# Optimization experiments

Measured on AMD Instinct MI355X. Metric: run time of the kernel, lower is better.

The kernel has to match this reference:

```python
import jax, jax.numpy as jnp
import numpy as np


def _ifft2c(k):
    # centered orthonormal 2D inverse FFT over axes (0, 1)
    return jnp.fft.fftshift(
        jnp.fft.ifft2(jnp.fft.ifftshift(k, axes=(0, 1)), axes=(0, 1), norm='ortho'),
        axes=(0, 1))


def _warp_adjoint(im, flow):
    # Adjoint (transpose) of bilinear-interpolation motion matrix built from a
    # 2D displacement field: scatter-add each pixel's value to the 4 bilinear
    # neighbors of its displaced location (x+u, y+v).
    # im: [Nx, Ny] complex64, flow: [Nx, Ny, 2] float32
    Nx, Ny = im.shape
    X, Y = jnp.meshgrid(jnp.arange(Nx, dtype=flow.dtype),
                        jnp.arange(Ny, dtype=flow.dtype), indexing='ij')
    px = jnp.clip(X + flow[..., 0], 0.0, Nx - 1.0)
    py = jnp.clip(Y + flow[..., 1], 0.0, Ny - 1.0)
    x0 = jnp.floor(px).astype(jnp.int32)
    y0 = jnp.floor(py).astype(jnp.int32)
    x1 = jnp.minimum(x0 + 1, Nx - 1)
    y1 = jnp.minimum(y0 + 1, Ny - 1)
    wx = px - x0.astype(px.dtype)
    wy = py - y0.astype(py.dtype)
    out = jnp.zeros(Nx * Ny, dtype=im.dtype)
    for xi, yi, w in ((x0, y0, (1 - wx) * (1 - wy)),
                      (x0, y1, (1 - wx) * wy),
                      (x1, y0, wx * (1 - wy)),
                      (x1, y1, wx * wy)):
        out = out.at[(xi * Ny + yi).ravel()].add((w * im).ravel())
    return out.reshape(Nx, Ny)


def setup_inputs() -> dict:
    key = jax.random.key(0)
    k1, k2, k3, k4, k5, k6 = jax.random.split(key, 6)
    Nx, Ny, Nc, Nt = 320, 320, 16, 25
    kspace_r = jax.random.normal(k1, (Nx, Ny, Nc), dtype=jnp.float32)
    kspace_i = jax.random.normal(k2, (Nx, Ny, Nc), dtype=jnp.float32)
    # binary undersampling mask per coil per frame
    mask = jnp.round(jax.random.uniform(k3, (Nx, Ny, Nc, Nt), dtype=jnp.float32))
    smaps_r = jax.random.normal(k4, (Nx, Ny, Nc), dtype=jnp.float32)
    smaps_i = jax.random.normal(k5, (Nx, Ny, Nc), dtype=jnp.float32)
    # displacement fields, a few pixels of motion
    flow = 3.0 * jax.random.normal(k6, (Nx, Ny, 2, Nt), dtype=jnp.float32)
    return {'kspace_r': kspace_r, 'kspace_i': kspace_i, 'mask': mask,
            'smaps_r': smaps_r, 'smaps_i': smaps_i, 'flow': flow}


def reference(kspace_r, kspace_i, mask, smaps_r, smaps_i, flow):
    kspace = jax.lax.complex(kspace_r, kspace_i)          # [Nx,Ny,Nc]
    smaps = jax.lax.complex(smaps_r, smaps_i)             # [Nx,Ny,Nc]
    # per-frame masked k-space -> per-coil images: [Nx,Ny,Nc,Nt]
    km = kspace[:, :, :, None] * mask.astype(kspace.dtype)
    coil_ims = _ifft2c(km)
    # coil combine with conjugate sensitivities: [Nx,Ny,Nt]
    im_aux = jnp.sum(coil_ims * jnp.conj(smaps)[:, :, :, None], axis=2)
    # adjoint motion warp per frame, then sum over frames
    ims_t = jnp.moveaxis(im_aux, -1, 0)                   # [Nt,Nx,Ny]
    flows_t = jnp.moveaxis(flow, -1, 0)                   # [Nt,Nx,Ny,2]
    warped = jax.vmap(_warp_adjoint)(ims_t, flows_t)      # [Nt,Nx,Ny]
    out = jnp.sum(warped, axis=0)                         # [Nx,Ny] complex
    return jnp.stack([out.real, out.imag], axis=-1)       # [Nx,Ny,2] float32
```

## Files before the change

kernel.cpp:

```cpp
#include <hip/hip_runtime.h>
#include <hip/hip_fp16.h>


#define NX 320
#define NT 25
#define NC 16
#define BR 32
#define WH 16
static const float INV320 = 1.0f / 320.0f;

typedef float v2f __attribute__((ext_vector_type(2)));
typedef unsigned int u32;

__device__ __forceinline__ int rev6(int l) {
  return ((l & 1) << 5) | ((l & 2) << 3) | ((l & 4) << 1) |
         ((l & 8) >> 1) | ((l & 16) >> 3) | ((l & 32) >> 5);
}

__device__ __forceinline__ u32 h2u(__half2 h) {
  return *reinterpret_cast<u32*>(&h);
}
__device__ __forceinline__ __half2 u2h(u32 u) {
  return *reinterpret_cast<__half2*>(&u);
}
__device__ __forceinline__ __half2 swap16(__half2 h) {
  u32 u = h2u(h);
  u = (u >> 16) | (u << 16);
  return u2h(u);
}

template <int M>
__device__ __forceinline__ u32 lxoru(u32 x) {
  if constexpr (M == 1) {
    return (u32)__builtin_amdgcn_mov_dpp((int)x, 0xB1, 0xF, 0xF, true);
  } else if constexpr (M == 2) {
    return (u32)__builtin_amdgcn_mov_dpp((int)x, 0x4E, 0xF, 0xF, true);
  } else if constexpr (M == 32) {
    return (u32)__shfl_xor((int)x, 32);
  } else {
    constexpr int pat = (M << 10) | 0x1F;
    return (u32)__builtin_amdgcn_ds_swizzle((int)x, pat);
  }
}

struct TwH {
  __half2 sg[5], c2[5], s2n[5];
  __half2 sg5;
  __half2 w5c[4], w5s[4];
  __half2 C1h, C2h, S1h, nS1h, S2h, NP;
};

__device__ __forceinline__ void make_twh(int lane, TwH& tw) {
#pragma unroll
  for (int st = 0; st < 5; ++st) {
    int m = 32 >> st;
    bool bot = (lane & m) != 0;
    int j = lane & (m - 1);
    float ang = 3.14159265358979323846f * (float)j / (float)m;
    float s, c;
    __sincosf(ang, &s, &c);
    float g = bot ? -1.f : 1.f;
    float cc = bot ? c : 1.f, ss = bot ? s : 0.f;
    tw.sg[st] = __floats2half2_rn(g, g);
    tw.c2[st] = __floats2half2_rn(cc, cc);
    tw.s2n[st] = __floats2half2_rn(-ss, ss);
  }
  float g5 = (lane & 1) ? -1.f : 1.f;
  tw.sg5 = __floats2half2_rn(g5, g5);
  int k1 = rev6(lane);
  float b = (6.283185307179586f / 320.0f) * (float)k1;
  float s1, c1;
  __sincosf(b, &s1, &c1);
  float cq = 1.f, sq = 0.f;
#pragma unroll
  for (int q = 1; q < 5; ++q) {
    float nc = cq * c1 - sq * s1, ns = cq * s1 + sq * c1;
    cq = nc;
    sq = ns;
    tw.w5c[q - 1] = __floats2half2_rn(cq, cq);
    tw.w5s[q - 1] = __floats2half2_rn(-sq, sq);
  }
  const float C1 = 0.30901699437494742f, S1 = 0.95105651629515357f;
  const float C2 = -0.80901699437494742f, S2 = 0.58778525229247312f;
  tw.C1h = __floats2half2_rn(C1, C1);
  tw.C2h = __floats2half2_rn(C2, C2);
  tw.S1h = __floats2half2_rn(S1, S1);
  tw.nS1h = __floats2half2_rn(-S1, -S1);
  tw.S2h = __floats2half2_rn(S2, S2);
  tw.NP = __floats2half2_rn(-1.f, 1.f);
}

__device__ __forceinline__ __half2 cmul_h(__half2 t, __half2 c2, __half2 s2n) {
  return __hfma2(s2n, swap16(t), __hmul2(c2, t));
}

template <int M>
__device__ __forceinline__ void bstage_h(__half2 z[5], __half2 sg, __half2 c2,
                                         __half2 s2n) {
#pragma unroll
  for (int q = 0; q < 5; ++q) {
    __half2 o = u2h(lxoru<M>(h2u(z[q])));
    __half2 t = __hfma2(sg, z[q], o);
    z[q] = cmul_h(t, c2, s2n);
  }
}

__device__ __forceinline__ void fft320h(__half2 z[5], const TwH& tw) {
  bstage_h<32>(z, tw.sg[0], tw.c2[0], tw.s2n[0]);
  bstage_h<16>(z, tw.sg[1], tw.c2[1], tw.s2n[1]);
  bstage_h<8>(z, tw.sg[2], tw.c2[2], tw.s2n[2]);
  bstage_h<4>(z, tw.sg[3], tw.c2[3], tw.s2n[3]);
  bstage_h<2>(z, tw.sg[4], tw.c2[4], tw.s2n[4]);
  {
    __half2 o = u2h(lxoru<1>(h2u(z[0])));
    z[0] = __hfma2(tw.sg5, z[0], o);
#pragma unroll
    for (int q = 1; q < 5; ++q) {
      o = u2h(lxoru<1>(h2u(z[q])));
      __half2 t = __hfma2(tw.sg5, z[q], o);
      z[q] = cmul_h(t, tw.w5c[q - 1], tw.w5s[q - 1]);
    }
  }
  __half2 t0 = z[0], t1 = z[1], t2 = z[2], t3 = z[3], t4 = z[4];
  __half2 a1 = __hadd2(t1, t4), b1 = __hsub2(t1, t4);
  __half2 a2 = __hadd2(t2, t3), b2 = __hsub2(t2, t3);
  z[0] = __hadd2(t0, __hadd2(a1, a2));
  __half2 p = __hfma2(tw.C2h, a2, __hfma2(tw.C1h, a1, t0));
  __half2 q_ = __hfma2(tw.S2h, b2, __hmul2(tw.S1h, b1));
  __half2 r = __hfma2(tw.C1h, a2, __hfma2(tw.C2h, a1, t0));
  __half2 u = __hfma2(tw.nS1h, b2, __hmul2(tw.S2h, b1));
  __half2 qi = __hmul2(tw.NP, swap16(q_));
  __half2 ui = __hmul2(tw.NP, swap16(u));
  z[1] = __hadd2(p, qi);
  z[4] = __hsub2(p, qi);
  z[2] = __hadd2(r, ui);
  z[3] = __hsub2(r, ui);
}

__global__ __launch_bounds__(256) void prep_k(
    const float* __restrict__ mask, const float* __restrict__ kr,
    const float* __restrict__ ki, const float* __restrict__ sr,
    const float* __restrict__ si, const float* __restrict__ fl,
    unsigned int* __restrict__ mp, float2* __restrict__ kT,
    __half2* __restrict__ sT, float2* __restrict__ fs,
    float* __restrict__ out_f) {
  __shared__ __align__(16) char shmem[7552];
  int bid = blockIdx.x, tid = threadIdx.x;
  if (bid < 6400) {
    int xt = bid / 320, y = bid % 320;
    int w = tid >> 6, lane = tid & 63;
    float4* stage4 = (float4*)shmem;
    float* stage = (float*)shmem;
    unsigned int* tileu = (unsigned int*)(shmem + 6400);
#pragma unroll
    for (int k = 0; k < 4; ++k) {
      int xx = w * 4 + k;
      const float4* src =
          (const float4*)(mask + ((size_t)((xt * 16 + xx) * NX) + y) * (NC * NT));
      float4* dst4 = stage4 + w * 100;
      if (lane < 50) {
        dst4[lane] = src[lane];
        dst4[lane + 50] = src[lane + 50];
      }
      if (lane < 16) {
        const float* row = stage + w * 400 + lane * NT;
        unsigned int bits = 0;
#pragma unroll
        for (int t = 0; t < NT; ++t) bits |= (row[t] != 0.f) ? (1u << t) : 0u;
        tileu[xx * 17 + lane] = bits;
      }
    }
    __syncthreads();
    int c2 = tid >> 4, xx2 = tid & 15;
    mp[((size_t)(c2 * NX + y)) * NX + xt * 16 + xx2] = tileu[xx2 * 17 + c2];
  } else if (bid < 12800) {
    int r = bid - 6400;
    int xt = r % 20, y = r / 20;
    int xx = tid >> 4, c = tid & 15;
    float2* tilef = (float2*)shmem;
    size_t si_ = (size_t)((xt * 16 + xx) * NX + y) * NC + c;
    tilef[xx * 17 + c] = make_float2(kr[si_], ki[si_]);
    __syncthreads();
    int c2 = tid >> 4, xx2 = tid & 15;
    kT[((size_t)(c2 * NX + y)) * NX + xt * 16 + xx2] = tilef[xx2 * 17 + c2];
  } else if (bid < 19200) {
    int r = bid - 12800;
    int yt = r % 20, x = r / 20;
    int yy = tid >> 4, c = tid & 15;
    float2* tiles = (float2*)shmem;
    size_t si_ = (size_t)(x * NX + yt * 16 + yy) * NC + c;
    tiles[yy * 17 + c] = make_float2(sr[si_], si[si_]);
    __syncthreads();
    int c2 = tid >> 4, yy2 = tid & 15;
    float2 v = tiles[yy2 * 17 + c2];
    float sg = (yy2 & 1) ? -1.f : 1.f;
    sT[((size_t)(c2 * NX + x)) * NX + yt * 16 + yy2] =
        __floats2half2_rn(v.x * sg, v.y * sg);
  } else if (bid < 22400) {
    int r = bid - 19200;
    int nyt = r % 10, nx = r / 10;
    float* buf = (float*)shmem;
    size_t base = (size_t)(nx * NX + nyt * 32) * (2 * NT);
    const float2* src2 = (const float2*)(fl + base);
    float2* buf2 = (float2*)shmem;
    for (int f = tid; f < 800; f += 256) buf2[f] = src2[f];
    __syncthreads();
    for (int f = tid; f < 1600; f += 256) {
      int t = f / 64;
      int k = f % 64;
      int nyl = k >> 1, d = k & 1;
      size_t di = ((size_t)(t * NX + nx) * NX + nyt * 32 + nyl) * 2 + d;
      ((float*)fs)[di] = buf[(nyl * 2 + d) * NT + t];
    }
  } else {
    int idx = (bid - 22400) * 256 + tid;
    ((float4*)out_f)[idx] = make_float4(0.f, 0.f, 0.f, 0.f);
  }
}

__global__ __launch_bounds__(256) void pass1_k(
    const float2* __restrict__ kT, const unsigned int* __restrict__ mp,
    __half2* __restrict__ tmp, int c0) {
  int y = blockIdx.x, cg = blockIdx.y, c = c0 + cg;
  int tid = threadIdx.x, lane = tid & 63, w = tid >> 6;
  __half2 v[5];
  unsigned int mb[5];
  size_t rowbase = ((size_t)c * NX + y) * NX;
#pragma unroll
  for (int q = 0; q < 5; ++q) {
    int x = 5 * lane + q;
    float2 kv = kT[rowbase + x];
    float sg = ((lane + q) & 1) ? -INV320 : INV320;
    v[q] = __floats2half2_rn(kv.x * sg, kv.y * sg);
    mb[q] = mp[rowbase + x];
  }
  TwH tw;
  make_twh(lane, tw);
  int r6 = rev6(lane);
  float osg = ((lane & 32) ? -1.f : 1.f) * ((y & 1) ? -1.f : 1.f);
  __half2 osg2 = __floats2half2_rn(osg, osg);
  for (int t = w; t < NT; t += 4) {
    __half2 z[5];
#pragma unroll
    for (int q = 0; q < 5; ++q)
      z[q] = u2h(((mb[q] >> t) & 1u) ? h2u(v[q]) : 0u);
    fft320h(z, tw);
    __half2* dst = tmp + ((size_t)(cg * NT + t) * NX + y) * NX;
#pragma unroll
    for (int k2 = 0; k2 < 5; ++k2) dst[r6 + 64 * k2] = __hmul2(osg2, z[k2]);
  }
}

__global__ __launch_bounds__(256) void pass2_k(
    const __half2* __restrict__ tmp, const __half2* __restrict__ sT,
    __half2* __restrict__ im_aux, int c0, int G, int first) {
  int bx = blockIdx.x, t = blockIdx.y;
  int nxt_ = (bx >> 3) + 10 * (bx & 7);
  int tid = threadIdx.x, lane = tid & 63, j = tid >> 6;
  int nx = nxt_ * 4 + j;
  int k1 = rev6(lane);
  TwH tw;
  make_twh(lane, tw);
  __shared__ __half2 tile[2][NX][5];
  v2f acc[5] = {{0, 0}, {0, 0}, {0, 0}, {0, 0}, {0, 0}};

  int off[5], lw[5];
#pragma unroll
  for (int q = 0; q < 5; ++q) {
    int f = tid + q * 256;
    off[q] = (f >> 2) * NX + (f & 3);
    lw[q] = (f >> 2) * 5 + (f & 3);
  }
  const size_t pstride = (size_t)NT * NX * NX;
  const __half2* sbase = tmp + (size_t)t * NX * NX + nxt_ * 4;
  __half2* lds = &tile[0][0][0];

  __half2 nb[5];
#pragma unroll
  for (int q = 0; q < 5; ++q) nb[q] = sbase[off[q]];

  for (int cg = 0; cg < G; ++cg) {
    __half2 cb[5];
#pragma unroll
    for (int q = 0; q < 5; ++q) cb[q] = nb[q];
    if (cg + 1 < G) {
      const __half2* s = sbase + (size_t)(cg + 1) * pstride;
#pragma unroll
      for (int q = 0; q < 5; ++q) nb[q] = s[off[q]];
    }
    __half2* buf = lds + (cg & 1) * (NX * 5);
#pragma unroll
    for (int q = 0; q < 5; ++q) buf[lw[q]] = cb[q];
    const __half2* srow = sT + ((size_t)(c0 + cg) * NX + nx) * NX;
    __half2 smh[5];
#pragma unroll
    for (int k2 = 0; k2 < 5; ++k2) smh[k2] = srow[k1 + 64 * k2];
    __syncthreads();
    __half2 z[5];
#pragma unroll
    for (int q = 0; q < 5; ++q) z[q] = buf[(5 * lane + q) * 5 + j];
    fft320h(z, tw);
#pragma unroll
    for (int k2 = 0; k2 < 5; ++k2) {
      float2 sm = __half22float2(smh[k2]);
      float2 zf = __half22float2(z[k2]);
      v2f zv = {zf.x, zf.y};
      v2f zc = {zf.y, -zf.x};
      acc[k2] += sm.x * zv + sm.y * zc;
    }
  }
  __half2* dst = im_aux + ((size_t)t * NX + nx) * NX;
#pragma unroll
  for (int k2 = 0; k2 < 5; ++k2) {
    int ny = k1 + 64 * k2;
    v2f nv = acc[k2];
    if (!first) {
      float2 old = __half22float2(dst[ny]);
      nv.x += old.x;
      nv.y += old.y;
    }
    dst[ny] = __floats2half2_rn(nv.x, nv.y);
  }
}

__global__ __launch_bounds__(1024) void scatter_k(
    const __half2* __restrict__ im, const float2* __restrict__ fs,
    __half2* __restrict__ out_p, float* __restrict__ out_f, int nseg) {
  int b = blockIdx.x, seg = blockIdx.y, t = blockIdx.z;
  int r0 = b * BR;
  int tid = threadIdx.x, lane = tid & 63, w = tid >> 6;
  __shared__ __half2 acc[BR * NX];
  const __half2 h2z = __floats2half2_rn(0.f, 0.f);
  for (int i = tid; i < BR * NX; i += 1024) acc[i] = h2z;
  __syncthreads();
  int lo = max(r0 - WH, 0), hi = min(r0 + BR + WH, NX);
  int stride = 16 * nseg;
  for (int nx = lo + seg * 16 + w; nx < hi; nx += stride) {
    bool own = (nx >= r0) && (nx < r0 + BR);
    const __half2* imrow = im + ((size_t)t * NX + nx) * NX;
    const float2* frow = fs + ((size_t)t * NX + nx) * NX;
#pragma unroll
    for (int q = 0; q < 5; ++q) {
      int ny = lane + 64 * q;
      float2 v = __half22float2(imrow[ny]);
      float2 fl = frow[ny];
      float px = fminf(fmaxf((float)nx + fl.x, 0.f), 319.f);
      float py = fminf(fmaxf((float)ny + fl.y, 0.f), 319.f);
      int x0 = (int)floorf(px), y0 = (int)floorf(py);
      int x1 = min(x0 + 1, NX - 1), y1 = min(y0 + 1, NX - 1);
      float wx = px - (float)x0, wy = py - (float)y0;
      float w00 = (1.f - wx) * (1.f - wy), w01 = (1.f - wx) * wy;
      float w10 = wx * (1.f - wy), w11 = wx * wy;
#pragma unroll
      for (int half = 0; half < 2; ++half) {
        int r = half ? x1 : x0;
        float wa = half ? w10 : w00;
        float wb = half ? w11 : w01;
        if (r >= r0 && r < r0 + BR) {
          unsafeAtomicAdd(&acc[(r - r0) * NX + y0],
                          __floats2half2_rn(wa * v.x, wa * v.y));
          unsafeAtomicAdd(&acc[(r - r0) * NX + y1],
                          __floats2half2_rn(wb * v.x, wb * v.y));
        } else if (own) {
          int rb = (r / BR) * BR;
          if (nx < rb - WH || nx >= rb + BR + WH) {
            unsafeAtomicAdd(&out_f[((size_t)r * NX + y0) * 2], wa * v.x);
            unsafeAtomicAdd(&out_f[((size_t)r * NX + y0) * 2 + 1], wa * v.y);
            unsafeAtomicAdd(&out_f[((size_t)r * NX + y1) * 2], wb * v.x);
            unsafeAtomicAdd(&out_f[((size_t)r * NX + y1) * 2 + 1], wb * v.y);
          }
        }
      }
    }
  }
  __syncthreads();
  __half2* dst = out_p + (size_t)(seg * NT + t) * NX * NX + (size_t)r0 * NX;
  for (int i = tid; i < BR * NX; i += 1024) dst[i] = acc[i];
}

__global__ __launch_bounds__(256) void reduce_k(
    const __half2* __restrict__ out_p, const float* __restrict__ out_f,
    float* __restrict__ out, int nslice) {
  const int n = NX * NX;
  int i = blockIdx.x * 256 + threadIdx.x;
  if (i >= n) return;
  float2 s = ((const float2*)out_f)[i];
  for (int k = 0; k < nslice; ++k) {
    float2 v = __half22float2(out_p[(size_t)k * n + i]);
    s.x += v.x;
    s.y += v.y;
  }
  ((float2*)out)[i] = s;
}

extern "C" void kernel_launch(void* const* d_in, const int* in_sizes, int n_in,
                              void* d_out, int out_size, void* d_ws,
                              size_t ws_size, hipStream_t stream) {
  const float* kr = (const float*)d_in[0];
  const float* ki = (const float*)d_in[1];
  const float* mask = (const float*)d_in[2];
  const float* sr = (const float*)d_in[3];
  const float* si = (const float*)d_in[4];
  const float* fl = (const float*)d_in[5];
  float* out = (float*)d_out;

  const size_t tmp1 = (size_t)NT * NX * NX * 4;
  const size_t kT_b = (size_t)NC * NX * NX * 8;
  const size_t sT_b = (size_t)NC * NX * NX * 4;
  const size_t fs_b = (size_t)NT * NX * NX * 8;
  const size_t mp_b = (size_t)NC * NX * NX * 4;
  const size_t ia_b = (size_t)NT * NX * NX * 4;
  const size_t of_b = (size_t)NX * NX * 8;
  const size_t op1 = (size_t)NT * NX * NX * 4;

  int NSEG = 2, G = 16;
  for (;;) {
    size_t fixed = kT_b + sT_b + fs_b + mp_b + ia_b + of_b + NSEG * op1;
    if (ws_size >= fixed + (size_t)G * tmp1) break;
    if (G > 1) { G >>= 1; continue; }
    if (NSEG > 1) { NSEG >>= 1; G = 16; continue; }
    break;
  }

  char* w = (char*)d_ws;
  __half2* tmp = (__half2*)w;    w += (size_t)G * tmp1;
  float2* kT = (float2*)w;       w += kT_b;
  __half2* sT = (__half2*)w;     w += sT_b;
  float2* fs = (float2*)w;       w += fs_b;
  __half2* im_aux = (__half2*)w; w += ia_b;
  __half2* out_p = (__half2*)w;  w += (size_t)NSEG * op1;
  float* out_f = (float*)w;      w += of_b;
  unsigned int* mp = (unsigned int*)w;

  prep_k<<<22600, 256, 0, stream>>>(mask, kr, ki, sr, si, fl, mp, kT, sT, fs,
                                    out_f);

  for (int c0 = 0; c0 < NC; c0 += G) {
    pass1_k<<<dim3(NX, G), 256, 0, stream>>>(kT, mp, tmp, c0);
    pass2_k<<<dim3(80, NT), 256, 0, stream>>>(tmp, sT, im_aux, c0, G,
                                              c0 == 0 ? 1 : 0);
  }
  scatter_k<<<dim3(NX / BR, NSEG, NT), 1024, 0, stream>>>(im_aux, fs, out_p,
                                                          out_f, NSEG);
  reduce_k<<<400, 256, 0, stream>>>(out_p, out_f, out, NSEG * NT);
}
```

Measured before the change: 256.1 us.

## Move smap/flow/zero prep into first pass1 launch and stream mask loads

New measurement: 246.6 us. 3.7% less time.

```diff
diff --git a/kernel.cpp b/kernel.cpp
--- a/kernel.cpp
+++ b/kernel.cpp
@@ -10,6 +10,7 @@
 static const float INV320 = 1.0f / 320.0f;
 
 typedef float v2f __attribute__((ext_vector_type(2)));
+typedef float nv4f __attribute__((ext_vector_type(4)));
 typedef unsigned int u32;
 
 __device__ __forceinline__ int rev6(int l) {
@@ -139,28 +140,25 @@
 
 __global__ __launch_bounds__(256) void prep_k(
     const float* __restrict__ mask, const float* __restrict__ kr,
-    const float* __restrict__ ki, const float* __restrict__ sr,
-    const float* __restrict__ si, const float* __restrict__ fl,
-    unsigned int* __restrict__ mp, float2* __restrict__ kT,
-    __half2* __restrict__ sT, float2* __restrict__ fs,
-    float* __restrict__ out_f) {
+    const float* __restrict__ ki, unsigned int* __restrict__ mp,
+    float2* __restrict__ kT) {
   __shared__ __align__(16) char shmem[7552];
   int bid = blockIdx.x, tid = threadIdx.x;
   if (bid < 6400) {
     int xt = bid / 320, y = bid % 320;
     int w = tid >> 6, lane = tid & 63;
-    float4* stage4 = (float4*)shmem;
+    nv4f* stage4 = (nv4f*)shmem;
     float* stage = (float*)shmem;
     unsigned int* tileu = (unsigned int*)(shmem + 6400);
 #pragma unroll
     for (int k = 0; k < 4; ++k) {
       int xx = w * 4 + k;
-      const float4* src =
-          (const float4*)(mask + ((size_t)((xt * 16 + xx) * NX) + y) * (NC * NT));
-      float4* dst4 = stage4 + w * 100;
+      const nv4f* src =
+          (const nv4f*)(mask + ((size_t)((xt * 16 + xx) * NX) + y) * (NC * NT));
+      nv4f* dst4 = stage4 + w * 100;
       if (lane < 50) {
-        dst4[lane] = src[lane];
-        dst4[lane + 50] = src[lane + 50];
+        dst4[lane] = __builtin_nontemporal_load(&src[lane]);
+        dst4[lane + 50] = __builtin_nontemporal_load(&src[lane + 50]);
       }
       if (lane < 16) {
         const float* row = stage + w * 400 + lane * NT;
@@ -173,7 +171,7 @@
     __syncthreads();
     int c2 = tid >> 4, xx2 = tid & 15;
     mp[((size_t)(c2 * NX + y)) * NX + xt * 16 + xx2] = tileu[xx2 * 17 + c2];
-  } else if (bid < 12800) {
+  } else {
     int r = bid - 6400;
     int xt = r % 20, y = r / 20;
     int xx = tid >> 4, c = tid & 15;
@@ -183,8 +181,49 @@
     __syncthreads();
     int c2 = tid >> 4, xx2 = tid & 15;
     kT[((size_t)(c2 * NX + y)) * NX + xt * 16 + xx2] = tilef[xx2 * 17 + c2];
-  } else if (bid < 19200) {
-    int r = bid - 12800;
+  }
+}
+
+__global__ __launch_bounds__(256) void pass1_k(
+    const float2* __restrict__ kT, const unsigned int* __restrict__ mp,
+    __half2* __restrict__ tmp, int c0, int G, const float* __restrict__ sr,
+    const float* __restrict__ si, const float* __restrict__ fl,
+    __half2* __restrict__ sT, float2* __restrict__ fs,
+    float* __restrict__ out_f) {
+  __shared__ __align__(16) char shmem[6528];
+  int bid = blockIdx.x, tid = threadIdx.x;
+  int fftN = NX * G;
+  if (bid < fftN) {
+    int y = bid % NX, cg = bid / NX, c = c0 + cg;
+    int lane = tid & 63, w = tid >> 6;
+    __half2 v[5];
+    unsigned int mb[5];
+    size_t rowbase = ((size_t)c * NX + y) * NX;
+#pragma unroll
+    for (int q = 0; q < 5; ++q) {
+      int x = 5 * lane + q;
+      float2 kv = kT[rowbase + x];
+      float sg = ((lane + q) & 1) ? -INV320 : INV320;
+      v[q] = __floats2half2_rn(kv.x * sg, kv.y * sg);
+      mb[q] = mp[rowbase + x];
+    }
+    TwH tw;
+    make_twh(lane, tw);
+    int r6 = rev6(lane);
+    float osg = ((lane & 32) ? -1.f : 1.f) * ((y & 1) ? -1.f : 1.f);
+    __half2 osg2 = __floats2half2_rn(osg, osg);
+    for (int t = w; t < NT; t += 4) {
+      __half2 z[5];
+#pragma unroll
+      for (int q = 0; q < 5; ++q)
+        z[q] = u2h(((mb[q] >> t) & 1u) ? h2u(v[q]) : 0u);
+      fft320h(z, tw);
+      __half2* dst = tmp + ((size_t)(cg * NT + t) * NX + y) * NX;
+#pragma unroll
+      for (int k2 = 0; k2 < 5; ++k2) dst[r6 + 64 * k2] = __hmul2(osg2, z[k2]);
+    }
+  } else if (bid < fftN + 6400) {
+    int r = bid - fftN;
     int yt = r % 20, x = r / 20;
     int yy = tid >> 4, c = tid & 15;
     float2* tiles = (float2*)shmem;
@@ -196,8 +235,8 @@
     float sg = (yy2 & 1) ? -1.f : 1.f;
     sT[((size_t)(c2 * NX + x)) * NX + yt * 16 + yy2] =
         __floats2half2_rn(v.x * sg, v.y * sg);
-  } else if (bid < 22400) {
-    int r = bid - 19200;
+  } else if (bid < fftN + 9600) {
+    int r = bid - fftN - 6400;
     int nyt = r % 10, nx = r / 10;
     float* buf = (float*)shmem;
     size_t base = (size_t)(nx * NX + nyt * 32) * (2 * NT);
@@ -213,41 +252,8 @@
       ((float*)fs)[di] = buf[(nyl * 2 + d) * NT + t];
     }
   } else {
-    int idx = (bid - 22400) * 256 + tid;
+    int idx = (bid - fftN - 9600) * 256 + tid;
     ((float4*)out_f)[idx] = make_float4(0.f, 0.f, 0.f, 0.f);
-  }
-}
-
-__global__ __launch_bounds__(256) void pass1_k(
-    const float2* __restrict__ kT, const unsigned int* __restrict__ mp,
-    __half2* __restrict__ tmp, int c0) {
-  int y = blockIdx.x, cg = blockIdx.y, c = c0 + cg;
-  int tid = threadIdx.x, lane = tid & 63, w = tid >> 6;
-  __half2 v[5];
-  unsigned int mb[5];
-  size_t rowbase = ((size_t)c * NX + y) * NX;
-#pragma unroll
-  for (int q = 0; q < 5; ++q) {
-    int x = 5 * lane + q;
-    float2 kv = kT[rowbase + x];
-    float sg = ((lane + q) & 1) ? -INV320 : INV320;
-    v[q] = __floats2half2_rn(kv.x * sg, kv.y * sg);
-    mb[q] = mp[rowbase + x];
-  }
-  TwH tw;
-  make_twh(lane, tw);
-  int r6 = rev6(lane);
-  float osg = ((lane & 32) ? -1.f : 1.f) * ((y & 1) ? -1.f : 1.f);
-  __half2 osg2 = __floats2half2_rn(osg, osg);
-  for (int t = w; t < NT; t += 4) {
-    __half2 z[5];
-#pragma unroll
-    for (int q = 0; q < 5; ++q)
-      z[q] = u2h(((mb[q] >> t) & 1u) ? h2u(v[q]) : 0u);
-    fft320h(z, tw);
-    __half2* dst = tmp + ((size_t)(cg * NT + t) * NX + y) * NX;
-#pragma unroll
-    for (int k2 = 0; k2 < 5; ++k2) dst[r6 + 64 * k2] = __hmul2(osg2, z[k2]);
   }
 }
 
@@ -432,11 +438,12 @@
   float* out_f = (float*)w;      w += of_b;
   unsigned int* mp = (unsigned int*)w;
 
-  prep_k<<<22600, 256, 0, stream>>>(mask, kr, ki, sr, si, fl, mp, kT, sT, fs,
-                                    out_f);
+  prep_k<<<12800, 256, 0, stream>>>(mask, kr, ki, mp, kT);
 
   for (int c0 = 0; c0 < NC; c0 += G) {
-    pass1_k<<<dim3(NX, G), 256, 0, stream>>>(kT, mp, tmp, c0);
+    int extra = (c0 == 0) ? 9800 : 0;
+    pass1_k<<<NX * G + extra, 256, 0, stream>>>(kT, mp, tmp, c0, G, sr, si,
+                                                fl, sT, fs, out_f);
     pass2_k<<<dim3(80, NT), 256, 0, stream>>>(tmp, sT, im_aux, c0, G,
                                               c0 == 0 ? 1 : 0);
   }
```
